# Optimization experiments

Hardware: AMD Instinct MI355X
Metric: run time of the kernel (lower is better)

The kernel has to match this reference:

```python
import jax, jax.numpy as jnp
import numpy as np

HID = 50  # HIDDEN_SIZE in source


def _lstm_step(x, h, c, W_ih, W_hh, b):
    # PyTorch LSTM cell: gates order i, f, g, o
    gates = x @ W_ih.T + h @ W_hh.T + b  # [B, 4H]
    i, f, g, o = jnp.split(gates, 4, axis=-1)
    i = jax.nn.sigmoid(i)
    f = jax.nn.sigmoid(f)
    g = jnp.tanh(g)
    o = jax.nn.sigmoid(o)
    c = f * c + i * g
    h = o * jnp.tanh(c)
    return h, c


def setup_inputs() -> dict:
    key = jax.random.key(0)
    ks = jax.random.split(key, 11)
    B, S = 2048, 512
    H, I, O = HID, 1, 1
    s = 1.0 / np.sqrt(H)
    u = lambda k, shp: jax.random.uniform(k, shp, jnp.float32, -s, s)
    return {
        "source": jax.random.normal(ks[0], (B, S, I), jnp.float32),
        "enc_W_ih": u(ks[1], (4 * H, I)),
        "enc_W_hh": u(ks[2], (4 * H, H)),
        "enc_b_ih": u(ks[3], (4 * H,)),
        "enc_b_hh": u(ks[4], (4 * H,)),
        "dec_W_ih": u(ks[5], (4 * H, O)),
        "dec_W_hh": u(ks[6], (4 * H, H)),
        "dec_b_ih": u(ks[7], (4 * H,)),
        "dec_b_hh": u(ks[8], (4 * H,)),
        "fc_W": u(ks[9], (O, H)),
        "fc_b": u(ks[10], (O,)),
        "target_len": 256,
    }


def reference(source, enc_W_ih, enc_W_hh, enc_b_ih, enc_b_hh,
              dec_W_ih, dec_W_hh, dec_b_ih, dec_b_hh, fc_W, fc_b,
              target_len):
    B = source.shape[0]
    H = enc_W_hh.shape[1]
    dt = source.dtype
    h0 = jnp.zeros((B, H), dt)
    c0 = jnp.zeros((B, H), dt)

    enc_b = enc_b_ih + enc_b_hh

    def enc_step(carry, x_t):
        h, c = carry
        h, c = _lstm_step(x_t, h, c, enc_W_ih, enc_W_hh, enc_b)
        return (h, c), None

    # scan over time: [S, B, 1]
    (h, c), _ = jax.lax.scan(enc_step, (h0, c0), jnp.swapaxes(source, 0, 1))

    dec_b = dec_b_ih + dec_b_hh
    x0 = jnp.zeros((B, source.shape[2]), dt)  # decoder_input = zeros

    def dec_step(carry, _):
        x, h, c = carry
        h, c = _lstm_step(x, h, c, dec_W_ih, dec_W_hh, dec_b)
        y = h @ fc_W.T + fc_b  # [B, 1]
        return (y, h, c), y  # feed output back as next input

    _, ys = jax.lax.scan(dec_step, (x0, h, c), None, length=target_len)
    return jnp.swapaxes(ys, 0, 1)  # [B, target_len, 1]
```

## Files before the change

### kernel.cpp

```cpp
#include <hip/hip_runtime.h>


#define HID 50
#define SEQ 512
#define TGT 256
#define MB  4
#define L2E 1.44269504088896341f

typedef __attribute__((ext_vector_type(8))) short short8;
typedef __attribute__((ext_vector_type(4))) float f32x4;

__device__ __forceinline__ unsigned short f2bf(float f) {
    unsigned u = __float_as_uint(f);
    return (unsigned short)((u + 0x7fffu + ((u >> 16) & 1u)) >> 16);
}
__device__ __forceinline__ float bf2f(unsigned short b) {
    return __uint_as_float(((unsigned)b) << 16);
}
__device__ __forceinline__ float sigm2(float a) {
    return __builtin_amdgcn_rcpf(1.0f + __builtin_amdgcn_exp2f(-a));
}
__device__ __forceinline__ float tanhc(float c) {
    return fmaf(2.0f,
        __builtin_amdgcn_rcpf(1.0f + __builtin_amdgcn_exp2f(-2.0f * L2E * c)),
        -1.0f);
}

#define MFMA(A, B, C) __builtin_amdgcn_mfma_f32_16x16x32_bf16((A), (B), (C), 0, 0, 0)

#define HB(s, kt, qg) ((((s) * 2 + (kt)) * 4 + (qg)) * 32)
#define HFSZ (2 * 2 * 4 * 32)

#define GCORE(XK, HIN, HOUT)                                           \
    float hv;                                                          \
    {                                                                  \
        const short* hin_ = (HIN);                                     \
        short8 a00 = *(const short8*)(hin_ + HB(0, 0, kg) + bsel * 8); \
        short8 a01 = *(const short8*)(hin_ + HB(1, 0, kg) + bsel * 8); \
        short8 a10 = *(const short8*)(hin_ + HB(0, 1, kg) + bsel * 8); \
        short8 a11 = *(const short8*)(hin_ + HB(1, 1, kg) + bsel * 8); \
        float i0 = fmaf(wx[0], (XK), bb[0]);                           \
        float i1 = fmaf(wx[1], (XK), bb[1]);                           \
        float i2 = fmaf(wx[2], (XK), bb[2]);                           \
        float i3 = fmaf(wx[3], (XK), bb[3]);                           \
        f32x4 ac0 = {i0, i0, i0, i0};                                  \
        f32x4 ac1 = {i1, i1, i1, i1};                                  \
        f32x4 ac2 = {i2, i2, i2, i2};                                  \
        f32x4 ac3 = {i3, i3, i3, i3};                                  \
        ac0 = MFMA(a00, Bf[0][0][0], ac0);                             \
        ac1 = MFMA(a00, Bf[1][0][0], ac1);                             \
        ac2 = MFMA(a00, Bf[2][0][0], ac2);                             \
        ac3 = MFMA(a00, Bf[3][0][0], ac3);                             \
        ac0 = MFMA(a00, Bf[0][0][1], ac0);                             \
        ac1 = MFMA(a00, Bf[1][0][1], ac1);                             \
        ac2 = MFMA(a00, Bf[2][0][1], ac2);                             \
        ac3 = MFMA(a00, Bf[3][0][1], ac3);                             \
        ac0 = MFMA(a01, Bf[0][0][0], ac0);                             \
        ac1 = MFMA(a01, Bf[1][0][0], ac1);                             \
        ac2 = MFMA(a01, Bf[2][0][0], ac2);                             \
        ac3 = MFMA(a01, Bf[3][0][0], ac3);                             \
        ac0 = MFMA(a10, Bf[0][1][0], ac0);                             \
        ac1 = MFMA(a10, Bf[1][1][0], ac1);                             \
        ac2 = MFMA(a10, Bf[2][1][0], ac2);                             \
        ac3 = MFMA(a10, Bf[3][1][0], ac3);                             \
        ac0 = MFMA(a10, Bf[0][1][1], ac0);                             \
        ac1 = MFMA(a10, Bf[1][1][1], ac1);                             \
        ac2 = MFMA(a10, Bf[2][1][1], ac2);                             \
        ac3 = MFMA(a10, Bf[3][1][1], ac3);                             \
        ac0 = MFMA(a11, Bf[0][1][0], ac0);                             \
        ac1 = MFMA(a11, Bf[1][1][0], ac1);                             \
        ac2 = MFMA(a11, Bf[2][1][0], ac2);                             \
        ac3 = MFMA(a11, Bf[3][1][0], ac3);                             \
        float vi = sigm2(ac0[0]);                                      \
        float vf = sigm2(ac1[0]);                                      \
        float vg = fmaf(2.0f, sigm2(ac2[0]), -1.0f);                   \
        float vo = sigm2(ac3[0]);                                      \
        cc = fmaf(vf, cc, vi * vg);                                    \
        hv = vo * tanhc(cc);                                           \
        unsigned short q0 = f2bf(hv);                                  \
        unsigned short q1 = f2bf(hv - bf2f(q0));                       \
        short* ho_ = (HOUT);                                           \
        ho_[wr0] = (short)q0;                                          \
        ho_[wr1] = (short)q1;                                          \
    }

#define DSTEP(T, HIN, HOUT, PB)                                        \
    {                                                                  \
        GCORE(xc, HIN, HOUT)                                           \
        float p = fcw * hv;                                            \
        p += __shfl_xor(p, 1, 64);                                     \
        p += __shfl_xor(p, 2, 64);                                     \
        p += __shfl_xor(p, 4, 64);                                     \
        p += __shfl_xor(p, 8, 64);                                     \
        if (nl == 0) (PB)[kg * 4 + w] = p;                             \
        __syncthreads();                                               \
        f32x4 s_ = *(const f32x4*)&(PB)[kg * 4];                       \
        float y = s_[0] + s_[1] + s_[2] + s_[3] + fb;                  \
        if (w == 0 && nl == 0) out[(size_t)(b0 + kg) * TGT + (T)] = y; \
        xc = y;                                                        \
    }

extern "C" __global__ void __launch_bounds__(256, 2)
seq2seq_kernel(const float* __restrict__ src,
               const float* __restrict__ eWih, const float* __restrict__ eWhh,
               const float* __restrict__ eBih, const float* __restrict__ eBhh,
               const float* __restrict__ dWih, const float* __restrict__ dWhh,
               const float* __restrict__ dBih, const float* __restrict__ dBhh,
               const float* __restrict__ fcW, const float* __restrict__ fcB,
               float* __restrict__ out) {
    const int tid  = threadIdx.x;
    const int lane = tid & 63;
    const int w    = tid >> 6;
    const int nl   = lane & 15;
    const int kg   = lane >> 4;
    const int bsel = nl >> 2;
    const int un   = 16 * w + nl;
    const int b0   = blockIdx.x * MB;
    const int ukt  = un >> 5, uqg = (un >> 3) & 3, uj = un & 7;
    const int wr0  = HB(0, ukt, uqg) + kg * 8 + uj;
    const int wr1  = HB(1, ukt, uqg) + kg * 8 + uj;

    __shared__ __align__(16) short hfA[HFSZ], hfB[HFSZ];
    __shared__ __align__(16) float srcT[SEQ * MB];
    __shared__ __align__(16) float pbA[16], pbB[16];

    for (int i = tid; i < HFSZ; i += 256) { hfA[i] = 0; hfB[i] = 0; }
    for (int i = tid; i < SEQ * MB; i += 256) {
        int e = i >> 9, t = i & 511;
        srcT[t * MB + e] = src[(size_t)(b0 + e) * SEQ + t];
    }

    short8 Bf[4][2][2];
    float bb[4], wx[4];
    float cc = 0.0f;

    auto loadW = [&](const float* Wih, const float* Whh,
                     const float* Bih, const float* Bhh) {
#pragma unroll
        for (int g = 0; g < 4; ++g) {
            const float sc = (g == 2) ? 2.0f * L2E : L2E;
            const bool nv  = (un < HID);
            const int row  = g * HID + (nv ? un : 0);
            bb[g] = nv ? (Bih[row] + Bhh[row]) * sc : 0.0f;
            wx[g] = nv ? Wih[row] * sc : 0.0f;
#pragma unroll
            for (int kt = 0; kt < 2; ++kt) {
                short8 s0, s1;
#pragma unroll
                for (int j = 0; j < 8; ++j) {
                    int kk = kt * 32 + kg * 8 + j;
                    float wv = (nv && kk < HID)
                             ? Whh[(size_t)row * HID + kk] * sc : 0.0f;
                    unsigned short h0 = f2bf(wv);
                    unsigned short h1 = f2bf(wv - bf2f(h0));
                    s0[j] = (short)h0; s1[j] = (short)h1;
                }
                Bf[g][kt][0] = s0; Bf[g][kt][1] = s1;
            }
        }
    };

    loadW(eWih, eWhh, eBih, eBhh);
    __syncthreads();
    for (int t = 0; t < SEQ; t += 2) {
        { GCORE(srcT[t * MB + kg], hfA, hfB) }
        __syncthreads();
        { GCORE(srcT[(t + 1) * MB + kg], hfB, hfA) }
        __syncthreads();
    }

    loadW(dWih, dWhh, dBih, dBhh);
    const float fcw = (un < HID) ? fcW[un] : 0.0f;
    const float fb  = fcB[0];
    float xc = 0.0f;
    for (int t = 0; t < TGT; t += 2) {
        DSTEP(t,     hfA, hfB, pbA)
        DSTEP(t + 1, hfB, hfA, pbB)
    }
}

extern "C" void kernel_launch(void* const* d_in, const int* in_sizes, int n_in,
                              void* d_out, int out_size, void* d_ws, size_t ws_size,
                              hipStream_t stream) {
    const float* src  = (const float*)d_in[0];
    const float* eWih = (const float*)d_in[1];
    const float* eWhh = (const float*)d_in[2];
    const float* eBih = (const float*)d_in[3];
    const float* eBhh = (const float*)d_in[4];
    const float* dWih = (const float*)d_in[5];
    const float* dWhh = (const float*)d_in[6];
    const float* dBih = (const float*)d_in[7];
    const float* dBhh = (const float*)d_in[8];
    const float* fcW  = (const float*)d_in[9];
    const float* fcB  = (const float*)d_in[10];
    float* out = (float*)d_out;

    const int B = in_sizes[0] / SEQ;
    seq2seq_kernel<<<B / MB, 256, 0, stream>>>(src, eWih, eWhh, eBih, eBhh,
                                               dWih, dWhh, dBih, dBhh,
                                               fcW, fcB, out);
}
```

Baseline: 531.2 us.

## Run each 4-sequence LSTM group in a single wavefront without block barriers

```diff
diff --git a/kernel.cpp b/kernel.cpp
--- a/kernel.cpp
+++ b/kernel.cpp
@@ -5,6 +5,7 @@
 #define SEQ 512
 #define TGT 256
 #define MB  4
+#define NT  16
 #define L2E 1.44269504088896341f
 
 typedef __attribute__((ext_vector_type(8))) short short8;
@@ -28,79 +29,62 @@
 
 #define MFMA(A, B, C) __builtin_amdgcn_mfma_f32_16x16x32_bf16((A), (B), (C), 0, 0, 0)
 
-#define HB(s, kt, qg) ((((s) * 2 + (kt)) * 4 + (qg)) * 32)
-#define HFSZ (2 * 2 * 4 * 32)
-
-#define GCORE(XK, HIN, HOUT)                                           \
-    float hv;                                                          \
-    {                                                                  \
-        const short* hin_ = (HIN);                                     \
-        short8 a00 = *(const short8*)(hin_ + HB(0, 0, kg) + bsel * 8); \
-        short8 a01 = *(const short8*)(hin_ + HB(1, 0, kg) + bsel * 8); \
-        short8 a10 = *(const short8*)(hin_ + HB(0, 1, kg) + bsel * 8); \
-        short8 a11 = *(const short8*)(hin_ + HB(1, 1, kg) + bsel * 8); \
-        float i0 = fmaf(wx[0], (XK), bb[0]);                           \
-        float i1 = fmaf(wx[1], (XK), bb[1]);                           \
-        float i2 = fmaf(wx[2], (XK), bb[2]);                           \
-        float i3 = fmaf(wx[3], (XK), bb[3]);                           \
-        f32x4 ac0 = {i0, i0, i0, i0};                                  \
-        f32x4 ac1 = {i1, i1, i1, i1};                                  \
-        f32x4 ac2 = {i2, i2, i2, i2};                                  \
-        f32x4 ac3 = {i3, i3, i3, i3};                                  \
-        ac0 = MFMA(a00, Bf[0][0][0], ac0);                             \
-        ac1 = MFMA(a00, Bf[1][0][0], ac1);                             \
-        ac2 = MFMA(a00, Bf[2][0][0], ac2);                             \
-        ac3 = MFMA(a00, Bf[3][0][0], ac3);                             \
-        ac0 = MFMA(a00, Bf[0][0][1], ac0);                             \
-        ac1 = MFMA(a00, Bf[1][0][1], ac1);                             \
-        ac2 = MFMA(a00, Bf[2][0][1], ac2);                             \
-        ac3 = MFMA(a00, Bf[3][0][1], ac3);                             \
-        ac0 = MFMA(a01, Bf[0][0][0], ac0);                             \
-        ac1 = MFMA(a01, Bf[1][0][0], ac1);                             \
-        ac2 = MFMA(a01, Bf[2][0][0], ac2);                             \
-        ac3 = MFMA(a01, Bf[3][0][0], ac3);                             \
-        ac0 = MFMA(a10, Bf[0][1][0], ac0);                             \
-        ac1 = MFMA(a10, Bf[1][1][0], ac1);                             \
-        ac2 = MFMA(a10, Bf[2][1][0], ac2);                             \
-        ac3 = MFMA(a10, Bf[3][1][0], ac3);                             \
-        ac0 = MFMA(a10, Bf[0][1][1], ac0);                             \
-        ac1 = MFMA(a10, Bf[1][1][1], ac1);                             \
-        ac2 = MFMA(a10, Bf[2][1][1], ac2);                             \
-        ac3 = MFMA(a10, Bf[3][1][1], ac3);                             \
-        ac0 = MFMA(a11, Bf[0][1][0], ac0);                             \
-        ac1 = MFMA(a11, Bf[1][1][0], ac1);                             \
-        ac2 = MFMA(a11, Bf[2][1][0], ac2);                             \
-        ac3 = MFMA(a11, Bf[3][1][0], ac3);                             \
-        float vi = sigm2(ac0[0]);                                      \
-        float vf = sigm2(ac1[0]);                                      \
-        float vg = fmaf(2.0f, sigm2(ac2[0]), -1.0f);                   \
-        float vo = sigm2(ac3[0]);                                      \
-        cc = fmaf(vf, cc, vi * vg);                                    \
-        hv = vo * tanhc(cc);                                           \
-        unsigned short q0 = f2bf(hv);                                  \
-        unsigned short q1 = f2bf(hv - bf2f(q0));                       \
-        short* ho_ = (HOUT);                                           \
-        ho_[wr0] = (short)q0;                                          \
-        ho_[wr1] = (short)q1;                                          \
+#define GSTEP(XV, IB, OB)                                                   \
+    {                                                                       \
+        const short* hp_ = &hs[IB][as][ab][0];                              \
+        short8 a0 = *(const short8*)(hp_ + kg * 8);           \
+        short8 a1 = *(const short8*)(hp_ + 32 + kg * 8);      \
+        float xv_ = (XV);                                                   \
+        f32x4 acc[NT];                                                      \
+        _Pragma("unroll")                                                   \
+        for (int j = 0; j < NT; ++j) {                                      \
+            f32x4 z = {0.0f, 0.0f, 0.0f, 0.0f};                             \
+            z = MFMA(a0, Bw[j][0][0], z);                                   \
+            z = MFMA(a0, Bw[j][0][1], z);                                   \
+            z = MFMA(a1, Bw[j][1][0], z);                                   \
+            z = MFMA(a1, Bw[j][1][1], z);                                   \
+            acc[j] = z;                                                     \
+        }                                                                   \
+        short* wp_ = &hs[OB][0][0][0];                                      \
+        _Pragma("unroll")                                                   \
+        for (int ug = 0; ug < 4; ++ug) {                                    \
+            float sI = acc[0 * 4 + ug][0] + acc[0 * 4 + ug][2]              \
+                     + fmaf(wx[0 * 4 + ug], xv_, bb[0 * 4 + ug]);           \
+            float sF = acc[1 * 4 + ug][0] + acc[1 * 4 + ug][2]              \
+                     + fmaf(wx[1 * 4 + ug], xv_, bb[1 * 4 + ug]);           \
+            float sG = acc[2 * 4 + ug][0] + acc[2 * 4 + ug][2]              \
+                     + fmaf(wx[2 * 4 + ug], xv_, bb[2 * 4 + ug]);           \
+            float sO = acc[3 * 4 + ug][0] + acc[3 * 4 + ug][2]              \
+                     + fmaf(wx[3 * 4 + ug], xv_, bb[3 * 4 + ug]);           \
+            float vi = sigm2(sI);                                           \
+            float vf = sigm2(sF);                                           \
+            float vg = fmaf(2.0f, sigm2(sG), -1.0f);                        \
+            float vo = sigm2(sO);                                           \
+            cc[ug] = fmaf(vf, cc[ug], vi * vg);                             \
+            hv[ug] = vo * tanhc(cc[ug]);                                    \
+            unsigned short q0 = f2bf(hv[ug]);                               \
+            unsigned short q1 = f2bf(hv[ug] - bf2f(q0));                    \
+            wp_[wofs + ug * 16]       = (short)q0;              \
+            wp_[wofs + ug * 16 + 288] = (short)q1;              \
+        }                                                                   \
     }
 
-#define DSTEP(T, HIN, HOUT, PB)                                        \
-    {                                                                  \
-        GCORE(xc, HIN, HOUT)                                           \
-        float p = fcw * hv;                                            \
-        p += __shfl_xor(p, 1, 64);                                     \
-        p += __shfl_xor(p, 2, 64);                                     \
-        p += __shfl_xor(p, 4, 64);                                     \
-        p += __shfl_xor(p, 8, 64);                                     \
-        if (nl == 0) (PB)[kg * 4 + w] = p;                             \
-        __syncthreads();                                               \
-        f32x4 s_ = *(const f32x4*)&(PB)[kg * 4];                       \
-        float y = s_[0] + s_[1] + s_[2] + s_[3] + fb;                  \
-        if (w == 0 && nl == 0) out[(size_t)(b0 + kg) * TGT + (T)] = y; \
-        xc = y;                                                        \
+#define DSTEP(T, IB, OB)                                                    \
+    {                                                                       \
+        GSTEP(xc, IB, OB)                                                   \
+        float p = fmaf(fcw0, hv[0],                                         \
+                  fmaf(fcw1, hv[1],                                         \
+                  fmaf(fcw2, hv[2], fcw3 * hv[3])));                        \
+        p += __shfl_xor(p, 1);                                              \
+        p += __shfl_xor(p, 2);                                              \
+        p += __shfl_xor(p, 4);                                              \
+        p += __shfl_xor(p, 8);                                              \
+        float y = p + fb;                                                   \
+        if (c == 0) ys[kg][T] = y;                                          \
+        xc = y;                                                             \
     }
 
-extern "C" __global__ void __launch_bounds__(256, 2)
+extern "C" __global__ void __launch_bounds__(64, 1)
 seq2seq_kernel(const float* __restrict__ src,
                const float* __restrict__ eWih, const float* __restrict__ eWhh,
                const float* __restrict__ eBih, const float* __restrict__ eBhh,
@@ -108,74 +92,78 @@
                const float* __restrict__ dBih, const float* __restrict__ dBhh,
                const float* __restrict__ fcW, const float* __restrict__ fcB,
                float* __restrict__ out) {
-    const int tid  = threadIdx.x;
-    const int lane = tid & 63;
-    const int w    = tid >> 6;
-    const int nl   = lane & 15;
+    const int lane = threadIdx.x & 63;
+    const int c    = lane & 15;
     const int kg   = lane >> 4;
-    const int bsel = nl >> 2;
-    const int un   = 16 * w + nl;
+    const int ab   = c >> 2;
+    const int as   = (c >> 1) & 1;
     const int b0   = blockIdx.x * MB;
-    const int ukt  = un >> 5, uqg = (un >> 3) & 3, uj = un & 7;
-    const int wr0  = HB(0, ukt, uqg) + kg * 8 + uj;
-    const int wr1  = HB(1, ukt, uqg) + kg * 8 + uj;
+    const int wofs = kg * 72 + c;
 
-    __shared__ __align__(16) short hfA[HFSZ], hfB[HFSZ];
+    __shared__ __align__(16) short hs[2][2][MB][72];
     __shared__ __align__(16) float srcT[SEQ * MB];
-    __shared__ __align__(16) float pbA[16], pbB[16];
+    __shared__ __align__(16) float ys[MB][TGT];
 
-    for (int i = tid; i < HFSZ; i += 256) { hfA[i] = 0; hfB[i] = 0; }
-    for (int i = tid; i < SEQ * MB; i += 256) {
+    for (int i = lane; i < 2 * 2 * MB * 72 / 2; i += 64) ((int*)hs)[i] = 0;
+    for (int i = lane; i < SEQ * MB; i += 64) {
         int e = i >> 9, t = i & 511;
         srcT[t * MB + e] = src[(size_t)(b0 + e) * SEQ + t];
     }
 
-    short8 Bf[4][2][2];
-    float bb[4], wx[4];
-    float cc = 0.0f;
+    short8 Bw[NT][2][2];
+    float wx[NT], bb[NT];
+    float cc[4] = {0.0f, 0.0f, 0.0f, 0.0f};
+    float hv[4];
 
     auto loadW = [&](const float* Wih, const float* Whh,
                      const float* Bih, const float* Bhh) {
 #pragma unroll
-        for (int g = 0; g < 4; ++g) {
+        for (int j = 0; j < NT; ++j) {
+            const int g  = j >> 2, ug = j & 3;
+            const int u  = ug * 16 + c;
+            const bool uv = (u < HID);
             const float sc = (g == 2) ? 2.0f * L2E : L2E;
-            const bool nv  = (un < HID);
-            const int row  = g * HID + (nv ? un : 0);
-            bb[g] = nv ? (Bih[row] + Bhh[row]) * sc : 0.0f;
-            wx[g] = nv ? Wih[row] * sc : 0.0f;
+            const int row = g * HID + (uv ? u : 0);
+            wx[j] = uv ? Wih[row] * sc : 0.0f;
+            bb[j] = uv ? (Bih[row] + Bhh[row]) * sc : 0.0f;
 #pragma unroll
             for (int kt = 0; kt < 2; ++kt) {
                 short8 s0, s1;
 #pragma unroll
-                for (int j = 0; j < 8; ++j) {
-                    int kk = kt * 32 + kg * 8 + j;
-                    float wv = (nv && kk < HID)
+                for (int jj = 0; jj < 8; ++jj) {
+                    int kk = kt * 32 + kg * 8 + jj;
+                    float wv = (uv && kk < HID)
                              ? Whh[(size_t)row * HID + kk] * sc : 0.0f;
                     unsigned short h0 = f2bf(wv);
-                    unsigned short h1 = f2bf(wv - bf2f(h0));
-                    s0[j] = (short)h0; s1[j] = (short)h1;
+                    s0[jj] = (short)h0;
+                    s1[jj] = (short)f2bf(wv - bf2f(h0));
                 }
-                Bf[g][kt][0] = s0; Bf[g][kt][1] = s1;
+                Bw[j][kt][0] = s0; Bw[j][kt][1] = s1;
             }
         }
     };
 
     loadW(eWih, eWhh, eBih, eBhh);
-    __syncthreads();
     for (int t = 0; t < SEQ; t += 2) {
-        { GCORE(srcT[t * MB + kg], hfA, hfB) }
-        __syncthreads();
-        { GCORE(srcT[(t + 1) * MB + kg], hfB, hfA) }
-        __syncthreads();
+        { GSTEP(srcT[t * MB + kg], 0, 1) }
+        { GSTEP(srcT[(t + 1) * MB + kg], 1, 0) }
     }
 
     loadW(dWih, dWhh, dBih, dBhh);
-    const float fcw = (un < HID) ? fcW[un] : 0.0f;
-    const float fb  = fcB[0];
+    const float fcw0 = fcW[c];
+    const float fcw1 = fcW[16 + c];
+    const float fcw2 = fcW[32 + c];
+    const float fcw3 = (48 + c < HID) ? fcW[48 + c] : 0.0f;
+    const float fb   = fcB[0];
     float xc = 0.0f;
     for (int t = 0; t < TGT; t += 2) {
-        DSTEP(t,     hfA, hfB, pbA)
-        DSTEP(t + 1, hfB, hfA, pbB)
+        DSTEP(t,     0, 1)
+        DSTEP(t + 1, 1, 0)
+    }
+
+    for (int i = lane; i < MB * TGT; i += 64) {
+        int b = i >> 8, t = i & 255;
+        out[(size_t)(b0 + b) * TGT + t] = ys[b][t];
     }
 }
 
@@ -196,7 +184,7 @@
     float* out = (float*)d_out;
 
     const int B = in_sizes[0] / SEQ;
-    seq2seq_kernel<<<B / MB, 256, 0, stream>>>(src, eWih, eWhh, eBih, eBhh,
-                                               dWih, dWhh, dBih, dBhh,
-                                               fcW, fcB, out);
+    seq2seq_kernel<<<B / MB, 64, 0, stream>>>(src, eWih, eWhh, eBih, eBhh,
+                                              dWih, dWhh, dBih, dBhh,
+                                              fcW, fcB, out);
 }
```

After: 893.1 us. 1.68x slower.
